# Optimization experiments

Hardware: AMD Instinct MI355X
Metric: run time of the kernel (lower is better)

Reference implementation:

```python
import jax, jax.numpy as jnp
import numpy as np


def setup_inputs() -> dict:
    key = jax.random.key(0)
    k1, k2, k3 = jax.random.split(key, 3)
    N, E, D = 100000, 3200000, 32  # neurons, total edges (fan-in sum), feature dim
    src = jax.random.normal(k1, (N, D), dtype=jnp.float32)
    gather_idx = jax.random.randint(k2, (E,), 0, N, dtype=jnp.int32)
    # repeat_interleave(arange(N), repeats) is nondecreasing -> sorted segment ids
    segment_ids = jnp.sort(jax.random.randint(k3, (E,), 0, N, dtype=jnp.int32))
    return {"src": src, "gather_idx": gather_idx, "segment_ids": segment_ids, "num_segments": N}


def reference(src, gather_idx, segment_ids, num_segments):
    # gather neuron input values: [E, D]
    gathered = src[gather_idx]
    # scatter_mean over variable-length groups (segment mean)
    sums = jax.ops.segment_sum(gathered, segment_ids, num_segments=num_segments,
                               indices_are_sorted=True)
    counts = jax.ops.segment_sum(jnp.ones((gathered.shape[0],), dtype=src.dtype),
                                 segment_ids, num_segments=num_segments,
                                 indices_are_sorted=True)
    return sums / jnp.maximum(counts, 1.0)[:, None]
```

## Files before the change

kernel.cpp:

```cpp
#include <hip/hip_runtime.h>
#include <hip/hip_fp16.h>


constexpr int D = 32;
constexpr int HD = 16;
constexpr int GSZ = 2;
constexpr int BLOCK = 256;
constexpr int SEGS_PER_BLOCK = BLOCK / GSZ;

typedef _Float16 half8 __attribute__((ext_vector_type(8)));

__global__ __launch_bounds__(BLOCK) void prep_kernel(
    const float* __restrict__ src,
    const int*   __restrict__ segid,
    int*         __restrict__ start,
    _Float16*    __restrict__ hsrcA,
    _Float16*    __restrict__ hsrcB,
    int E, int N)
{
    const int t = blockIdx.x * BLOCK + threadIdx.x;

    if (t <= E) {
        int s, p;
        if (t == E) { s = N; p = segid[E - 1]; }
        else        { s = segid[t]; p = (t == 0) ? -1 : segid[t - 1]; }
        for (int n = p + 1; n <= s; ++n) start[n] = t;
    }

    if (t < 2 * N) {
        const int  row  = (t < N) ? t : t - N;
        const int  hoff = (t < N) ? 0 : HD;
        _Float16*  dst  = (t < N) ? hsrcA : hsrcB;
        const float* sp = src + (size_t)row * D + hoff;
        const float4 a = *(const float4*)(sp);
        const float4 b = *(const float4*)(sp + 4);
        const float4 c = *(const float4*)(sp + 8);
        const float4 d = *(const float4*)(sp + 12);
        half8 h0, h1;
        h0[0] = (_Float16)a.x; h0[1] = (_Float16)a.y; h0[2] = (_Float16)a.z; h0[3] = (_Float16)a.w;
        h0[4] = (_Float16)b.x; h0[5] = (_Float16)b.y; h0[6] = (_Float16)b.z; h0[7] = (_Float16)b.w;
        h1[0] = (_Float16)c.x; h1[1] = (_Float16)c.y; h1[2] = (_Float16)c.z; h1[3] = (_Float16)c.w;
        h1[4] = (_Float16)d.x; h1[5] = (_Float16)d.y; h1[6] = (_Float16)d.z; h1[7] = (_Float16)d.w;
        *(half8*)(dst + (size_t)row * HD)     = h0;
        *(half8*)(dst + (size_t)row * HD + 8) = h1;
    }
}

__global__ __launch_bounds__(BLOCK) void AggregationLayer_53051436040325_kernel(
    const _Float16* __restrict__ hsrcA,
    const _Float16* __restrict__ hsrcB,
    const int*      __restrict__ gidx,
    const int*      __restrict__ start,
    float*          __restrict__ out,
    int N, int nblkHalf)
{
    const int bid  = blockIdx.x;
    const int xcd  = bid & 7;
    const int hsel = xcd >> 2;
    const int wblk = (bid >> 3) * 4 + (xcd & 3);
    if (wblk >= nblkHalf) return;

    const int n   = wblk * SEGS_PER_BLOCK + (threadIdx.x >> 1);
    const int sub = threadIdx.x & 1;
    if (n >= N) return;

    const int lo = start[n];
    const int hi = start[n + 1];

    const _Float16* sp = (hsel ? hsrcB : hsrcA) + sub * 8;

    float acc[8];
#pragma unroll
    for (int j = 0; j < 8; ++j) acc[j] = 0.f;

    int e = lo;
    for (; e + 8 <= hi; e += 8) {
        int g[8];
#pragma unroll
        for (int k = 0; k < 8; ++k) g[k] = gidx[e + k];
        half8 v[8];
#pragma unroll
        for (int k = 0; k < 8; ++k) v[k] = *(const half8*)(sp + (size_t)g[k] * HD);
#pragma unroll
        for (int k = 0; k < 8; ++k)
#pragma unroll
            for (int j = 0; j < 8; ++j) acc[j] += (float)v[k][j];
    }
    for (; e < hi; ++e) {
        const half8 v = *(const half8*)(sp + (size_t)gidx[e] * HD);
#pragma unroll
        for (int j = 0; j < 8; ++j) acc[j] += (float)v[j];
    }

    const int c = hi - lo;
    const float inv = 1.f / (float)(c > 0 ? c : 1);
    float4 r0, r1;
    r0.x = acc[0] * inv; r0.y = acc[1] * inv; r0.z = acc[2] * inv; r0.w = acc[3] * inv;
    r1.x = acc[4] * inv; r1.y = acc[5] * inv; r1.z = acc[6] * inv; r1.w = acc[7] * inv;
    float* op = out + (size_t)n * D + hsel * HD + sub * 8;
    *(float4*)(op)     = r0;
    *(float4*)(op + 4) = r1;
}

extern "C" void kernel_launch(void* const* d_in, const int* in_sizes, int n_in,
                              void* d_out, int out_size, void* d_ws, size_t ws_size,
                              hipStream_t stream) {
    const float* src   = (const float*)d_in[0];
    const int*   gidx  = (const int*)d_in[1];
    const int*   segid = (const int*)d_in[2];
    const int E = in_sizes[1];
    const int N = in_sizes[0] / D;

    char* ws = (char*)d_ws;
    int* start = (int*)ws;
    size_t off = ((size_t)(N + 1) * sizeof(int) + 255) & ~(size_t)255;
    _Float16* hsrcA = (_Float16*)(ws + off);
    off += ((size_t)N * HD * sizeof(_Float16) + 255) & ~(size_t)255;
    _Float16* hsrcB = (_Float16*)(ws + off);

    float* out = (float*)d_out;

    const int threadsA = (E + 1 > 2 * N) ? (E + 1) : (2 * N);
    const int blocksA = (threadsA + BLOCK - 1) / BLOCK;
    prep_kernel<<<blocksA, BLOCK, 0, stream>>>(src, segid, start, hsrcA, hsrcB, E, N);

    const int nblkHalf = (N + SEGS_PER_BLOCK - 1) / SEGS_PER_BLOCK;
    const int blocksB  = ((2 * nblkHalf + 7) / 8) * 8;
    AggregationLayer_53051436040325_kernel<<<blocksB, BLOCK, 0, stream>>>(
        hsrcA, hsrcB, gidx, start, out, N, nblkHalf);
}
```

Measured before the change: 140.4 us.

## Use persistent blocks with atomic work queues keyed by hardware XCC id

Replaces the static grid, which mapped half-tables to XCDs by assuming round-robin block dispatch, with a fixed grid of persistent blocks. Each block reads its XCC id from a hardware register, drains the matching half-table queue through an atomic counter, then helps with the other half. Index, start and output accesses become nontemporal. This aims for dynamic load balancing across uneven segment lengths and cache affinity that holds regardless of how blocks are dispatched, at the cost of an atomic and two barriers per claim.

Result: slower. 186.9 us (+33.1%).

```diff
diff --git a/kernel.cpp b/kernel.cpp
--- a/kernel.cpp
+++ b/kernel.cpp
@@ -2,23 +2,27 @@
 #include <hip/hip_fp16.h>
 
 
-constexpr int D = 32;
+constexpr int D  = 32;
 constexpr int HD = 16;
-constexpr int GSZ = 2;
 constexpr int BLOCK = 256;
-constexpr int SEGS_PER_BLOCK = BLOCK / GSZ;
+constexpr int SEGS_PER_CLAIM = BLOCK / 2;
+constexpr int GRID_MAIN = 2048;
 
 typedef _Float16 half8 __attribute__((ext_vector_type(8)));
+typedef float    f32x4 __attribute__((ext_vector_type(4)));
 
 __global__ __launch_bounds__(BLOCK) void prep_kernel(
     const float* __restrict__ src,
     const int*   __restrict__ segid,
+    int*         __restrict__ q,
     int*         __restrict__ start,
     _Float16*    __restrict__ hsrcA,
     _Float16*    __restrict__ hsrcB,
     int E, int N)
 {
     const int t = blockIdx.x * BLOCK + threadIdx.x;
+
+    if (t < 2) q[t] = 0;
 
     if (t <= E) {
         int s, p;
@@ -51,55 +55,71 @@
     const _Float16* __restrict__ hsrcB,
     const int*      __restrict__ gidx,
     const int*      __restrict__ start,
+    int*            __restrict__ q,
     float*          __restrict__ out,
-    int N, int nblkHalf)
+    int N)
 {
-    const int bid  = blockIdx.x;
-    const int xcd  = bid & 7;
-    const int hsel = xcd >> 2;
-    const int wblk = (bid >> 3) * 4 + (xcd & 3);
-    if (wblk >= nblkHalf) return;
+    __shared__ int s_c;
 
-    const int n   = wblk * SEGS_PER_BLOCK + (threadIdx.x >> 1);
-    const int sub = threadIdx.x & 1;
-    if (n >= N) return;
+    int xcc;
+    asm volatile("s_getreg_b32 %0, hwreg(HW_REG_XCC_ID)" : "=s"(xcc));
+    const int my = (xcc >> 2) & 1;
 
-    const int lo = start[n];
-    const int hi = start[n + 1];
+    const int segoff = threadIdx.x >> 1;
+    const int sub    = threadIdx.x & 1;
 
-    const _Float16* sp = (hsel ? hsrcB : hsrcA) + sub * 8;
+    for (int pass = 0; pass < 2; ++pass) {
+        const int h = my ^ pass;
+        const _Float16* __restrict__ table = h ? hsrcB : hsrcA;
+        int* qq = q + h;
 
-    float acc[8];
+        while (true) {
+            if (threadIdx.x == 0) s_c = atomicAdd(qq, 1);
+            __syncthreads();
+            const int n0 = s_c * SEGS_PER_CLAIM;
+            __syncthreads();
+            if (n0 >= N) break;
+
+            const int n = n0 + segoff;
+            if (n < N) {
+                const int lo = __builtin_nontemporal_load(start + n);
+                const int hi = __builtin_nontemporal_load(start + n + 1);
+                const _Float16* sp = table + sub * 8;
+
+                float acc[8];
 #pragma unroll
-    for (int j = 0; j < 8; ++j) acc[j] = 0.f;
+                for (int j = 0; j < 8; ++j) acc[j] = 0.f;
 
-    int e = lo;
-    for (; e + 8 <= hi; e += 8) {
-        int g[8];
+                int e = lo;
+                for (; e + 8 <= hi; e += 8) {
+                    int g[8];
 #pragma unroll
-        for (int k = 0; k < 8; ++k) g[k] = gidx[e + k];
-        half8 v[8];
+                    for (int k = 0; k < 8; ++k) g[k] = __builtin_nontemporal_load(gidx + e + k);
+                    half8 v[8];
 #pragma unroll
-        for (int k = 0; k < 8; ++k) v[k] = *(const half8*)(sp + (size_t)g[k] * HD);
+                    for (int k = 0; k < 8; ++k) v[k] = *(const half8*)(sp + (size_t)g[k] * HD);
 #pragma unroll
-        for (int k = 0; k < 8; ++k)
+                    for (int k = 0; k < 8; ++k)
 #pragma unroll
-            for (int j = 0; j < 8; ++j) acc[j] += (float)v[k][j];
+                        for (int j = 0; j < 8; ++j) acc[j] += (float)v[k][j];
+                }
+                for (; e < hi; ++e) {
+                    const int g = __builtin_nontemporal_load(gidx + e);
+                    const half8 v = *(const half8*)(sp + (size_t)g * HD);
+#pragma unroll
+                    for (int j = 0; j < 8; ++j) acc[j] += (float)v[j];
+                }
+
+                const int cnt = hi - lo;
+                const float inv = 1.f / (float)(cnt > 0 ? cnt : 1);
+                f32x4 r0 = { acc[0] * inv, acc[1] * inv, acc[2] * inv, acc[3] * inv };
+                f32x4 r1 = { acc[4] * inv, acc[5] * inv, acc[6] * inv, acc[7] * inv };
+                float* op = out + (size_t)n * D + h * HD + sub * 8;
+                __builtin_nontemporal_store(r0, (f32x4*)(op));
+                __builtin_nontemporal_store(r1, (f32x4*)(op + 4));
+            }
+        }
     }
-    for (; e < hi; ++e) {
-        const half8 v = *(const half8*)(sp + (size_t)gidx[e] * HD);
-#pragma unroll
-        for (int j = 0; j < 8; ++j) acc[j] += (float)v[j];
-    }
-
-    const int c = hi - lo;
-    const float inv = 1.f / (float)(c > 0 ? c : 1);
-    float4 r0, r1;
-    r0.x = acc[0] * inv; r0.y = acc[1] * inv; r0.z = acc[2] * inv; r0.w = acc[3] * inv;
-    r1.x = acc[4] * inv; r1.y = acc[5] * inv; r1.z = acc[6] * inv; r1.w = acc[7] * inv;
-    float* op = out + (size_t)n * D + hsel * HD + sub * 8;
-    *(float4*)(op)     = r0;
-    *(float4*)(op + 4) = r1;
 }
 
 extern "C" void kernel_launch(void* const* d_in, const int* in_sizes, int n_in,
@@ -112,8 +132,10 @@
     const int N = in_sizes[0] / D;
 
     char* ws = (char*)d_ws;
-    int* start = (int*)ws;
-    size_t off = ((size_t)(N + 1) * sizeof(int) + 255) & ~(size_t)255;
+    int* q = (int*)ws;
+    size_t off = 256;
+    int* start = (int*)(ws + off);
+    off += ((size_t)(N + 1) * sizeof(int) + 255) & ~(size_t)255;
     _Float16* hsrcA = (_Float16*)(ws + off);
     off += ((size_t)N * HD * sizeof(_Float16) + 255) & ~(size_t)255;
     _Float16* hsrcB = (_Float16*)(ws + off);
@@ -122,10 +144,8 @@
 
     const int threadsA = (E + 1 > 2 * N) ? (E + 1) : (2 * N);
     const int blocksA = (threadsA + BLOCK - 1) / BLOCK;
-    prep_kernel<<<blocksA, BLOCK, 0, stream>>>(src, segid, start, hsrcA, hsrcB, E, N);
+    prep_kernel<<<blocksA, BLOCK, 0, stream>>>(src, segid, q, start, hsrcA, hsrcB, E, N);
 
-    const int nblkHalf = (N + SEGS_PER_BLOCK - 1) / SEGS_PER_BLOCK;
-    const int blocksB  = ((2 * nblkHalf + 7) / 8) * 8;
-    AggregationLayer_53051436040325_kernel<<<blocksB, BLOCK, 0, stream>>>(
-        hsrcA, hsrcB, gidx, start, out, N, nblkHalf);
+    AggregationLayer_53051436040325_kernel<<<GRID_MAIN, BLOCK, 0, stream>>>(
+        hsrcA, hsrcB, gidx, start, q, out, N);
 }
```

## Interleave fp16 feature table and drop per-XCD half split in gather

Applied to the files above, without the earlier changes.

The fp16 copy of the source table now keeps each full 32-wide row contiguous, instead of two separate half-width tables that were routed to different XCD groups by block id. Each segment is handled by four threads, each owning 8 features, so every index is read once rather than once per half. Index loads are vectorized as int4 and use nontemporal hints, and the output stores are nontemporal. The cost is that each XCD's L2 now has to cache the whole 6.4MB table instead of half of it, so gather hit rates may drop. The int4 index loads are also not guaranteed to be 16-byte aligned.

Result: faster. 133.0 us (-5.3%).

```diff
diff --git a/kernel.cpp b/kernel.cpp
--- a/kernel.cpp
+++ b/kernel.cpp
@@ -2,20 +2,20 @@
 #include <hip/hip_fp16.h>
 
 
-constexpr int D = 32;
-constexpr int HD = 16;
-constexpr int GSZ = 2;
+constexpr int D  = 32;
+constexpr int GSZ = 4;
 constexpr int BLOCK = 256;
 constexpr int SEGS_PER_BLOCK = BLOCK / GSZ;
 
 typedef _Float16 half8 __attribute__((ext_vector_type(8)));
+typedef float    f32x4 __attribute__((ext_vector_type(4)));
+typedef int      int4a __attribute__((ext_vector_type(4)));
 
 __global__ __launch_bounds__(BLOCK) void prep_kernel(
     const float* __restrict__ src,
     const int*   __restrict__ segid,
     int*         __restrict__ start,
-    _Float16*    __restrict__ hsrcA,
-    _Float16*    __restrict__ hsrcB,
+    _Float16*    __restrict__ hsrc,
     int E, int N)
 {
     const int t = blockIdx.x * BLOCK + threadIdx.x;
@@ -28,9 +28,8 @@
     }
 
     if (t < 2 * N) {
-        const int  row  = (t < N) ? t : t - N;
-        const int  hoff = (t < N) ? 0 : HD;
-        _Float16*  dst  = (t < N) ? hsrcA : hsrcB;
+        const int row  = t >> 1;
+        const int hoff = (t & 1) * 16;
         const float* sp = src + (size_t)row * D + hoff;
         const float4 a = *(const float4*)(sp);
         const float4 b = *(const float4*)(sp + 4);
@@ -41,33 +40,27 @@
         h0[4] = (_Float16)b.x; h0[5] = (_Float16)b.y; h0[6] = (_Float16)b.z; h0[7] = (_Float16)b.w;
         h1[0] = (_Float16)c.x; h1[1] = (_Float16)c.y; h1[2] = (_Float16)c.z; h1[3] = (_Float16)c.w;
         h1[4] = (_Float16)d.x; h1[5] = (_Float16)d.y; h1[6] = (_Float16)d.z; h1[7] = (_Float16)d.w;
-        *(half8*)(dst + (size_t)row * HD)     = h0;
-        *(half8*)(dst + (size_t)row * HD + 8) = h1;
+        _Float16* dst = hsrc + (size_t)row * D + hoff;
+        *(half8*)(dst)     = h0;
+        *(half8*)(dst + 8) = h1;
     }
 }
 
 __global__ __launch_bounds__(BLOCK) void AggregationLayer_53051436040325_kernel(
-    const _Float16* __restrict__ hsrcA,
-    const _Float16* __restrict__ hsrcB,
+    const _Float16* __restrict__ hsrc,
     const int*      __restrict__ gidx,
     const int*      __restrict__ start,
     float*          __restrict__ out,
-    int N, int nblkHalf)
+    int N)
 {
-    const int bid  = blockIdx.x;
-    const int xcd  = bid & 7;
-    const int hsel = xcd >> 2;
-    const int wblk = (bid >> 3) * 4 + (xcd & 3);
-    if (wblk >= nblkHalf) return;
-
-    const int n   = wblk * SEGS_PER_BLOCK + (threadIdx.x >> 1);
-    const int sub = threadIdx.x & 1;
+    const int n   = blockIdx.x * SEGS_PER_BLOCK + (threadIdx.x >> 2);
+    const int sub = threadIdx.x & (GSZ - 1);
     if (n >= N) return;
 
-    const int lo = start[n];
-    const int hi = start[n + 1];
+    const int lo = __builtin_nontemporal_load(start + n);
+    const int hi = __builtin_nontemporal_load(start + n + 1);
 
-    const _Float16* sp = (hsel ? hsrcB : hsrcA) + sub * 8;
+    const _Float16* sp = hsrc + sub * 8;
 
     float acc[8];
 #pragma unroll
@@ -75,31 +68,32 @@
 
     int e = lo;
     for (; e + 8 <= hi; e += 8) {
-        int g[8];
-#pragma unroll
-        for (int k = 0; k < 8; ++k) g[k] = gidx[e + k];
+        const int4a ga = __builtin_nontemporal_load((const int4a*)(gidx + e));
+        const int4a gb = __builtin_nontemporal_load((const int4a*)(gidx + e + 4));
         half8 v[8];
 #pragma unroll
-        for (int k = 0; k < 8; ++k) v[k] = *(const half8*)(sp + (size_t)g[k] * HD);
+        for (int k = 0; k < 4; ++k) v[k]     = *(const half8*)(sp + (size_t)ga[k] * D);
+#pragma unroll
+        for (int k = 0; k < 4; ++k) v[k + 4] = *(const half8*)(sp + (size_t)gb[k] * D);
 #pragma unroll
         for (int k = 0; k < 8; ++k)
 #pragma unroll
             for (int j = 0; j < 8; ++j) acc[j] += (float)v[k][j];
     }
     for (; e < hi; ++e) {
-        const half8 v = *(const half8*)(sp + (size_t)gidx[e] * HD);
+        const int g = __builtin_nontemporal_load(gidx + e);
+        const half8 v = *(const half8*)(sp + (size_t)g * D);
 #pragma unroll
         for (int j = 0; j < 8; ++j) acc[j] += (float)v[j];
     }
 
     const int c = hi - lo;
     const float inv = 1.f / (float)(c > 0 ? c : 1);
-    float4 r0, r1;
-    r0.x = acc[0] * inv; r0.y = acc[1] * inv; r0.z = acc[2] * inv; r0.w = acc[3] * inv;
-    r1.x = acc[4] * inv; r1.y = acc[5] * inv; r1.z = acc[6] * inv; r1.w = acc[7] * inv;
-    float* op = out + (size_t)n * D + hsel * HD + sub * 8;
-    *(float4*)(op)     = r0;
-    *(float4*)(op + 4) = r1;
+    f32x4 r0 = { acc[0] * inv, acc[1] * inv, acc[2] * inv, acc[3] * inv };
+    f32x4 r1 = { acc[4] * inv, acc[5] * inv, acc[6] * inv, acc[7] * inv };
+    float* op = out + (size_t)n * D + sub * 8;
+    __builtin_nontemporal_store(r0, (f32x4*)(op));
+    __builtin_nontemporal_store(r1, (f32x4*)(op + 4));
 }
 
 extern "C" void kernel_launch(void* const* d_in, const int* in_sizes, int n_in,
@@ -114,18 +108,14 @@
     char* ws = (char*)d_ws;
     int* start = (int*)ws;
     size_t off = ((size_t)(N + 1) * sizeof(int) + 255) & ~(size_t)255;
-    _Float16* hsrcA = (_Float16*)(ws + off);
-    off += ((size_t)N * HD * sizeof(_Float16) + 255) & ~(size_t)255;
-    _Float16* hsrcB = (_Float16*)(ws + off);
+    _Float16* hsrc = (_Float16*)(ws + off);
 
     float* out = (float*)d_out;
 
     const int threadsA = (E + 1 > 2 * N) ? (E + 1) : (2 * N);
     const int blocksA = (threadsA + BLOCK - 1) / BLOCK;
-    prep_kernel<<<blocksA, BLOCK, 0, stream>>>(src, segid, start, hsrcA, hsrcB, E, N);
+    prep_kernel<<<blocksA, BLOCK, 0, stream>>>(src, segid, start, hsrc, E, N);
 
-    const int nblkHalf = (N + SEGS_PER_BLOCK - 1) / SEGS_PER_BLOCK;
-    const int blocksB  = ((2 * nblkHalf + 7) / 8) * 8;
-    AggregationLayer_53051436040325_kernel<<<blocksB, BLOCK, 0, stream>>>(
-        hsrcA, hsrcB, gidx, start, out, N, nblkHalf);
+    const int blocksB = (N + SEGS_PER_BLOCK - 1) / SEGS_PER_BLOCK;
+    AggregationLayer_53051436040325_kernel<<<blocksB, BLOCK, 0, stream>>>(hsrc, gidx, start, out, N);
 }
```
